# Performance work log

Measured on AMD Instinct MI355X. Metric: run time of the kernel, lower is better.

Reference implementation:

```python
import jax, jax.numpy as jnp
import numpy as np

B, S, D, H = 4, 2048, 1024, 16
DH = D // H
DFF = 4 * D
EPS = 1e-7


def _layernorm(x, scale, shift):
    # Note original quirk: (normalized + shift) * scale, biased variance, eps=1e-7
    m = jnp.mean(x, axis=-1, keepdims=True)
    v = jnp.mean((x - m) ** 2, axis=-1, keepdims=True)
    return ((x - m) / jnp.sqrt(v + EPS) + shift) * scale


def _gelu(x):
    c = jnp.sqrt(jnp.asarray(2.0 / jnp.pi, dtype=x.dtype))
    return 0.5 * x * (1.0 + jnp.tanh(c * (x + 0.044715 * x ** 3)))


def setup_inputs() -> dict:
    key = jax.random.key(0)
    ks = jax.random.split(key, 8)
    s = 0.02
    return {
        "x": jax.random.normal(ks[0], (B, S, D), jnp.float32),
        "Wq": jax.random.normal(ks[1], (D, D), jnp.float32) * s,
        "Wk": jax.random.normal(ks[2], (D, D), jnp.float32) * s,
        "Wv": jax.random.normal(ks[3], (D, D), jnp.float32) * s,
        "Wo": jax.random.normal(ks[4], (D, D), jnp.float32) * s,
        "bo": jnp.zeros((D,), jnp.float32),
        "W1": jax.random.normal(ks[5], (DFF, D), jnp.float32) * s,
        "b1": jnp.zeros((DFF,), jnp.float32),
        "W2": jax.random.normal(ks[6], (D, DFF), jnp.float32) * s,
        "b2": jnp.zeros((D,), jnp.float32),
        "ln1_scale": jnp.ones((D,), jnp.float32),
        "ln1_shift": jnp.zeros((D,), jnp.float32),
        "ln2_scale": jnp.ones((D,), jnp.float32),
        "ln2_shift": jnp.zeros((D,), jnp.float32),
    }


def reference(x, Wq, Wk, Wv, Wo, bo, W1, b1, W2, b2,
              ln1_scale, ln1_shift, ln2_scale, ln2_shift):
    b, s, d = x.shape
    h = _layernorm(x, ln1_scale, ln1_shift)
    # torch Linear: y = h @ W.T
    q = (h @ Wq.T).reshape(b, s, H, DH).transpose(0, 2, 1, 3)  # bhsd
    k = (h @ Wk.T).reshape(b, s, H, DH).transpose(0, 2, 1, 3)
    v = (h @ Wv.T).reshape(b, s, H, DH).transpose(0, 2, 1, 3)
    scores = jnp.einsum('bhqd,bhkd->bhqk', q, k) / jnp.sqrt(jnp.asarray(DH, x.dtype))
    causal = jnp.tril(jnp.ones((s, s), dtype=bool))
    scores = jnp.where(causal, scores, -jnp.inf)
    attn = jax.nn.softmax(scores, axis=-1)
    ctx = jnp.einsum('bhqk,bhkd->bhqd', attn, v)
    ctx = ctx.transpose(0, 2, 1, 3).reshape(b, s, d)
    attn_out = ctx @ Wo.T + bo
    x1 = x + attn_out  # residual (dropout is identity at eval / p effectively unused)
    h2 = _layernorm(x1, ln2_scale, ln2_shift)
    ff = _gelu(h2 @ W1.T + b1) @ W2.T + b2
    return x1 + ff
```

## Files before the change

kernel.cpp:

```cpp
#include <hip/hip_runtime.h>
#include <hip/hip_bf16.h>
#include <math.h>

typedef __bf16 bf16;
typedef __bf16 bf16x2_t __attribute__((ext_vector_type(2)));
typedef __bf16 bf16x4_t __attribute__((ext_vector_type(4)));
typedef __bf16 bf16x8_t __attribute__((ext_vector_type(8)));
typedef float  floatx4  __attribute__((ext_vector_type(4)));

#define DEVI static __device__ __forceinline__

constexpr int Bb = 4, Ss = 2048, Dd = 1024, Hh = 16, DHh = 64, DFFc = 4096;
constexpr int NTOK = Bb * Ss;
constexpr int NQKV = 3072;

DEVI void gld_lds16(const void* g, void* l) {
  __builtin_amdgcn_global_load_lds(
      (const __attribute__((address_space(1))) void*)g,
      (__attribute__((address_space(3))) void*)l, 16, 0, 0);
}

DEVI float gelu_f(float x) {
  const float c = 0.7978845608028654f;
  float t = tanhf(c * (x + 0.044715f * x * x * x));
  return 0.5f * x * (1.0f + t);
}

DEVI int xcd_lin(int lin, int nwg) {
  return (lin & 7) * (nwg >> 3) + (lin >> 3);
}

struct CastArgs {
  const float* src[6];
  bf16* dst[6];
  int n[6];
};
__global__ __launch_bounds__(256) void cast_w_kernel(CastArgs a) {
  const int which = blockIdx.y;
  const int idx = (blockIdx.x * 256 + threadIdx.x) * 4;
  if (idx >= a.n[which]) return;
  float4 v = *(const float4*)(a.src[which] + idx);
  bf16x4_t o = {(bf16)v.x, (bf16)v.y, (bf16)v.z, (bf16)v.w};
  *(bf16x4_t*)(a.dst[which] + idx) = o;
}

template <typename TIN>
__global__ __launch_bounds__(256) void ln_kernel(const TIN* __restrict__ x,
                                                 const float* __restrict__ sc,
                                                 const float* __restrict__ sh,
                                                 bf16* __restrict__ out) {
  __shared__ float rs[4], rs2[4];
  const int row = blockIdx.x, t = threadIdx.x;
  const TIN* xr = x + (size_t)row * Dd;
  float v[4];
  if constexpr (sizeof(TIN) == 2) {
    bf16x4_t tmp = *(const bf16x4_t*)((const bf16*)xr + t * 4);
#pragma unroll
    for (int i = 0; i < 4; i++) v[i] = (float)tmp[i];
  } else {
    float4 tmp = *(const float4*)((const float*)xr + t * 4);
    v[0] = tmp.x; v[1] = tmp.y; v[2] = tmp.z; v[3] = tmp.w;
  }
  float s = v[0] + v[1] + v[2] + v[3];
  float s2 = v[0] * v[0] + v[1] * v[1] + v[2] * v[2] + v[3] * v[3];
#pragma unroll
  for (int off = 1; off < 64; off <<= 1) {
    s += __shfl_xor(s, off);
    s2 += __shfl_xor(s2, off);
  }
  if ((t & 63) == 0) { rs[t >> 6] = s; rs2[t >> 6] = s2; }
  __syncthreads();
  float S1 = rs[0] + rs[1] + rs[2] + rs[3];
  float S2 = rs2[0] + rs2[1] + rs2[2] + rs2[3];
  float mean = S1 * (1.0f / Dd);
  float var = S2 * (1.0f / Dd) - mean * mean;
  float rinv = rsqrtf(var + 1e-7f);
#pragma unroll
  for (int i = 0; i < 4; i++) {
    int c = t * 4 + i;
    out[(size_t)row * Dd + c] = (bf16)(((v[i] - mean) * rinv + sh[c]) * sc[c]);
  }
}

template <int MODE>
__global__ __launch_bounds__(256) void gemm_bt(const bf16* __restrict__ A,
                                               const bf16* __restrict__ Bw,
                                               const float* __restrict__ bias,
                                               const void* __restrict__ res,
                                               void* __restrict__ outp,
                                               int M, int N, int K) {
  __shared__ bf16 As[128 * 32];
  __shared__ bf16 Bs[128 * 32];
  const int tid = threadIdx.x;
  const int gx = (int)gridDim.x;
  const int nwg = gx * (int)gridDim.y;
  const int lin = xcd_lin((int)blockIdx.y * gx + (int)blockIdx.x, nwg);
  const int m0 = (lin / gx) * 128;
  const int n0 = (lin % gx) * 128;
  const int wave = tid >> 6, lane = tid & 63;
  const int quad = lane >> 4, l16 = lane & 15;
  const int wm = (wave >> 1) * 64, wn = (wave & 1) * 64;

  floatx4 acc[4][4] = {};

  const int e0 = tid * 8;
  const int r0 = e0 >> 5, c0 = e0 & 31;
  const bf16* Ap0 = A + (size_t)(m0 + r0) * K + c0;
  const bf16* Ap1 = A + (size_t)(m0 + r0 + 64) * K + c0;
  const bf16* Bp0 = Bw + (size_t)(n0 + r0) * K + c0;
  const bf16* Bp1 = Bw + (size_t)(n0 + r0 + 64) * K + c0;

  for (int k = 0; k < K; k += 32) {
    __syncthreads();
    gld_lds16(Ap0 + k, As + e0);
    gld_lds16(Ap1 + k, As + e0 + 2048);
    gld_lds16(Bp0 + k, Bs + e0);
    gld_lds16(Bp1 + k, Bs + e0 + 2048);
    __syncthreads();

    bf16x8_t af[4], bfv[4];
#pragma unroll
    for (int i = 0; i < 4; i++) {
      af[i] = *(const bf16x8_t*)(As + (wm + i * 16 + l16) * 32 + quad * 8);
      bfv[i] = *(const bf16x8_t*)(Bs + (wn + i * 16 + l16) * 32 + quad * 8);
    }
#pragma unroll
    for (int i = 0; i < 4; i++)
#pragma unroll
      for (int j = 0; j < 4; j++)
        acc[i][j] =
            __builtin_amdgcn_mfma_f32_16x16x32_bf16(af[i], bfv[j], acc[i][j], 0, 0, 0);
  }

#pragma unroll
  for (int i = 0; i < 4; i++) {
    const int rbase = m0 + wm + i * 16 + quad * 4;
#pragma unroll
    for (int j = 0; j < 4; j++) {
      const int col = n0 + wn + j * 16 + l16;
      float bv = 0.f;
      if constexpr (MODE == 1 || MODE == 2 || MODE == 3) bv = bias[col];
#pragma unroll
      for (int r = 0; r < 4; r++) {
        const int row = rbase + r;
        float vacc = acc[i][j][r] + bv;
        if constexpr (MODE == 0) {
          ((bf16*)outp)[(size_t)row * N + col] = (bf16)vacc;
        } else if constexpr (MODE == 1) {
          float xres = ((const float*)res)[(size_t)row * N + col];
          ((bf16*)outp)[(size_t)row * N + col] = (bf16)(xres + vacc);
        } else if constexpr (MODE == 2) {
          ((bf16*)outp)[(size_t)row * N + col] = (bf16)gelu_f(vacc);
        } else {
          float xres = (float)((const bf16*)res)[(size_t)row * N + col];
          ((float*)outp)[(size_t)row * N + col] = xres + vacc;
        }
      }
    }
  }
}

__global__ __launch_bounds__(256) void attn_kernel(const bf16* __restrict__ QKV,
                                                   bf16* __restrict__ ctx) {
  __shared__ bf16 Ks[64 * 72];
  __shared__ bf16 Vt[64 * 72];
  __shared__ bf16 Ps[4][16 * 72];

  const int tid = threadIdx.x;
  const int wave = tid >> 6, lane = tid & 63;
  const int quad = lane >> 4, l16 = lane & 15;
  const int lin = xcd_lin((int)blockIdx.y * 16 + (int)blockIdx.x, 16 * Bb * Hh);
  const int qb = lin & 15;
  const int bh = lin >> 4;
  const int bsel = bh >> 4, hsel = bh & 15;
  const size_t base = ((size_t)bsel * Ss) * NQKV + (size_t)hsel * 64;
  const bf16* Qp = QKV + base;
  const bf16* Kp = QKV + base + 1024;
  const bf16* Vp = QKV + base + 2048;

  const int kr0 = tid >> 3, kc0 = (tid & 7) * 8;
  const int vp2 = tid & 31, vs = tid >> 5;

  for (int t = 0; t < 2; t++) {
    const int qt = (t == 0) ? qb : 31 - qb;
    const int q0 = qt * 64;

    const int qrow = q0 + wave * 16 + l16;
    bf16x8_t qf0 = *(const bf16x8_t*)(Qp + (size_t)qrow * NQKV + quad * 8);
    bf16x8_t qf1 = *(const bf16x8_t*)(Qp + (size_t)qrow * NQKV + 32 + quad * 8);
#pragma unroll
    for (int i = 0; i < 8; i++) {
      qf0[i] = (bf16)((float)qf0[i] * 0.125f);
      qf1[i] = (bf16)((float)qf1[i] * 0.125f);
    }

    floatx4 o[4] = {};
    float l_i[4] = {0.f, 0.f, 0.f, 0.f};

    for (int kc = 0; kc < q0 + 64; kc += 64) {
      __syncthreads();
      *(bf16x8_t*)(Ks + kr0 * 72 + kc0) =
          *(const bf16x8_t*)(Kp + (size_t)(kc + kr0) * NQKV + kc0);
      *(bf16x8_t*)(Ks + (kr0 + 32) * 72 + kc0) =
          *(const bf16x8_t*)(Kp + (size_t)(kc + kr0 + 32) * NQKV + kc0);
      {
        const bf16* v0p = Vp + (size_t)(kc + 2 * vp2) * NQKV + vs * 8;
        bf16x8_t va = *(const bf16x8_t*)(v0p);
        bf16x8_t vb = *(const bf16x8_t*)(v0p + NQKV);
#pragma unroll
        for (int i = 0; i < 8; i++) {
          bf16x2_t p2 = {va[i], vb[i]};
          *(bf16x2_t*)(Vt + (vs * 8 + i) * 72 + 2 * vp2) = p2;
        }
      }
      __syncthreads();

      floatx4 sg[4];
      __builtin_amdgcn_s_setprio(1);
#pragma unroll
      for (int g = 0; g < 4; g++) {
        floatx4 s = {0.f, 0.f, 0.f, 0.f};
        bf16x8_t ka = *(const bf16x8_t*)(Ks + (g * 16 + l16) * 72 + quad * 8);
        bf16x8_t kb = *(const bf16x8_t*)(Ks + (g * 16 + l16) * 72 + 32 + quad * 8);
        s = __builtin_amdgcn_mfma_f32_16x16x32_bf16(qf0, ka, s, 0, 0, 0);
        s = __builtin_amdgcn_mfma_f32_16x16x32_bf16(qf1, kb, s, 0, 0, 0);
        sg[g] = s;
      }
      __builtin_amdgcn_s_setprio(0);

      bf16* pw = &Ps[wave][0];
#pragma unroll
      for (int r = 0; r < 4; r++) {
        const int rq = q0 + wave * 16 + quad * 4 + r;
        float p[4];
        float rsum = 0.f;
#pragma unroll
        for (int g = 0; g < 4; g++) {
          float v = (kc + g * 16 + l16 > rq) ? -1e30f : sg[g][r];
          p[g] = __expf(v);
          rsum += p[g];
        }
        rsum += __shfl_xor(rsum, 1);
        rsum += __shfl_xor(rsum, 2);
        rsum += __shfl_xor(rsum, 4);
        rsum += __shfl_xor(rsum, 8);
        l_i[r] += rsum;
#pragma unroll
        for (int g = 0; g < 4; g++)
          pw[(quad * 4 + r) * 72 + g * 16 + l16] = (bf16)p[g];
      }
      __syncthreads();

      bf16x8_t pf0 = *(const bf16x8_t*)(pw + l16 * 72 + quad * 8);
      bf16x8_t pf1 = *(const bf16x8_t*)(pw + l16 * 72 + 32 + quad * 8);
      __builtin_amdgcn_s_setprio(1);
#pragma unroll
      for (int nt = 0; nt < 4; nt++) {
        bf16x8_t vf0 = *(const bf16x8_t*)(Vt + (nt * 16 + l16) * 72 + quad * 8);
        bf16x8_t vf1 = *(const bf16x8_t*)(Vt + (nt * 16 + l16) * 72 + 32 + quad * 8);
        o[nt] = __builtin_amdgcn_mfma_f32_16x16x32_bf16(pf0, vf0, o[nt], 0, 0, 0);
        o[nt] = __builtin_amdgcn_mfma_f32_16x16x32_bf16(pf1, vf1, o[nt], 0, 0, 0);
      }
      __builtin_amdgcn_s_setprio(0);
    }

#pragma unroll
    for (int nt = 0; nt < 4; nt++)
#pragma unroll
      for (int r = 0; r < 4; r++) {
        const int rq = q0 + wave * 16 + quad * 4 + r;
        size_t a = ((size_t)bsel * Ss + rq) * Dd + (size_t)hsel * DHh + nt * 16 + l16;
        ctx[a] = (bf16)(o[nt][r] / l_i[r]);
      }
  }
}

extern "C" void kernel_launch(void* const* d_in, const int* in_sizes, int n_in,
                              void* d_out, int out_size, void* d_ws, size_t ws_size,
                              hipStream_t stream) {
  (void)in_sizes; (void)n_in; (void)out_size; (void)ws_size;
  const float* x = (const float*)d_in[0];
  const float* Wq = (const float*)d_in[1];
  const float* Wk = (const float*)d_in[2];
  const float* Wv = (const float*)d_in[3];
  const float* Wo = (const float*)d_in[4];
  const float* bo = (const float*)d_in[5];
  const float* W1 = (const float*)d_in[6];
  const float* b1 = (const float*)d_in[7];
  const float* W2 = (const float*)d_in[8];
  const float* b2 = (const float*)d_in[9];
  const float* ln1s = (const float*)d_in[10];
  const float* ln1b = (const float*)d_in[11];
  const float* ln2s = (const float*)d_in[12];
  const float* ln2b = (const float*)d_in[13];

  char* wsb = (char*)d_ws;
  const size_t MB = 1024 * 1024;
  bf16* Wqb = (bf16*)(wsb);
  bf16* Wkb = (bf16*)(wsb + 2 * MB);
  bf16* Wvb = (bf16*)(wsb + 4 * MB);
  bf16* Wob = (bf16*)(wsb + 6 * MB);
  bf16* W1b = (bf16*)(wsb + 8 * MB);
  bf16* W2b = (bf16*)(wsb + 16 * MB);
  bf16* h   = (bf16*)(wsb + 24 * MB);
  bf16* qkv = (bf16*)(wsb + 40 * MB);
  bf16* ctx = (bf16*)(wsb + 88 * MB);
  bf16* x1  = (bf16*)(wsb + 104 * MB);
  bf16* h2  = ctx;
  bf16* ff1 = h;

  dim3 blk(256, 1, 1);

  CastArgs ca;
  ca.src[0] = Wq; ca.src[1] = Wk; ca.src[2] = Wv; ca.src[3] = Wo;
  ca.src[4] = W1; ca.src[5] = W2;
  ca.dst[0] = Wqb; ca.dst[1] = Wkb; ca.dst[2] = Wvb; ca.dst[3] = Wob;
  ca.dst[4] = W1b; ca.dst[5] = W2b;
  ca.n[0] = ca.n[1] = ca.n[2] = ca.n[3] = Dd * Dd;
  ca.n[4] = ca.n[5] = Dd * DFFc;
  cast_w_kernel<<<dim3((Dd * DFFc) / (256 * 4), 6, 1), blk, 0, stream>>>(ca);

  ln_kernel<float><<<dim3(NTOK, 1, 1), blk, 0, stream>>>(x, ln1s, ln1b, h);
  gemm_bt<0><<<dim3(24, NTOK / 128, 1), blk, 0, stream>>>(h, Wqb, nullptr, nullptr, qkv,
                                                          NTOK, NQKV, Dd);
  attn_kernel<<<dim3(16, Bb * Hh, 1), blk, 0, stream>>>(qkv, ctx);
  gemm_bt<1><<<dim3(8, NTOK / 128, 1), blk, 0, stream>>>(ctx, Wob, bo, x, x1, NTOK, Dd, Dd);
  ln_kernel<bf16><<<dim3(NTOK, 1, 1), blk, 0, stream>>>(x1, ln2s, ln2b, h2);
  gemm_bt<2><<<dim3(32, NTOK / 128, 1), blk, 0, stream>>>(h2, W1b, b1, nullptr, ff1, NTOK,
                                                          DFFc, Dd);
  gemm_bt<3><<<dim3(8, NTOK / 128, 1), blk, 0, stream>>>(ff1, W2b, b2, x1, (float*)d_out,
                                                         NTOK, Dd, DFFc);
}
```

Before: 558.1 us.

## Replace GEMMs with 8-wave double-buffered swizzled-LDS kernel using 256-row tiles

Replaces the simple 128x128, K=32 single-buffered GEMM with a 512-thread kernel using 256xBN tiles and K=64 steps. LDS is double-buffered so the next tile's global-to-LDS loads are issued in phases while MFMAs run on the current buffer. An XOR swizzle is applied to the LDS layout to avoid bank conflicts. Wave priority is raised around the MFMA blocks. The larger tiles and LDS footprint reduce occupancy and grid size, and the GEMMs for smaller N now launch fewer workgroups.

After: 521.9 us. -6.5%, faster.

```diff
diff --git a/kernel.cpp b/kernel.cpp
--- a/kernel.cpp
+++ b/kernel.cpp
@@ -82,68 +82,154 @@
   }
 }
 
-template <int MODE>
-__global__ __launch_bounds__(256) void gemm_bt(const bf16* __restrict__ A,
-                                               const bf16* __restrict__ Bw,
-                                               const float* __restrict__ bias,
-                                               const void* __restrict__ res,
-                                               void* __restrict__ outp,
-                                               int M, int N, int K) {
-  __shared__ bf16 As[128 * 32];
-  __shared__ bf16 Bs[128 * 32];
+template <int BN, int MODE>
+__global__ __launch_bounds__(512, 2) void gemm8(const bf16* __restrict__ A,
+                                                const bf16* __restrict__ Bw,
+                                                const float* __restrict__ bias,
+                                                const void* __restrict__ res,
+                                                void* __restrict__ outp,
+                                                int M, int N, int K) {
+  constexpr int WARPS_N = (BN == 256) ? 4 : 2;
+  constexpr int WR_H = (BN == 256) ? 128 : 64;
+  constexpr int M_rep = WR_H / 16;
+  constexpr int MPP = M_rep / 4;
+  constexpr int NBCH = BN / 128;
+  constexpr int BELEM = BN * 64;
+  __shared__ bf16 lds[32768 + 2 * BELEM];
+
   const int tid = threadIdx.x;
+  const int w = tid >> 6, lane = tid & 63;
+  const int quad = lane >> 4, l16 = lane & 15;
+  const int l7x8 = (lane & 7) << 3;
+  const int wr = w / WARPS_N, wc = w % WARPS_N;
+
   const int gx = (int)gridDim.x;
   const int nwg = gx * (int)gridDim.y;
   const int lin = xcd_lin((int)blockIdx.y * gx + (int)blockIdx.x, nwg);
-  const int m0 = (lin / gx) * 128;
-  const int n0 = (lin % gx) * 128;
-  const int wave = tid >> 6, lane = tid & 63;
-  const int quad = lane >> 4, l16 = lane & 15;
-  const int wm = (wave >> 1) * 64, wn = (wave & 1) * 64;
-
-  floatx4 acc[4][4] = {};
-
-  const int e0 = tid * 8;
-  const int r0 = e0 >> 5, c0 = e0 & 31;
-  const bf16* Ap0 = A + (size_t)(m0 + r0) * K + c0;
-  const bf16* Ap1 = A + (size_t)(m0 + r0 + 64) * K + c0;
-  const bf16* Bp0 = Bw + (size_t)(n0 + r0) * K + c0;
-  const bf16* Bp1 = Bw + (size_t)(n0 + r0 + 64) * K + c0;
-
-  for (int k = 0; k < K; k += 32) {
-    __syncthreads();
-    gld_lds16(Ap0 + k, As + e0);
-    gld_lds16(Ap1 + k, As + e0 + 2048);
-    gld_lds16(Bp0 + k, Bs + e0);
-    gld_lds16(Bp1 + k, Bs + e0 + 2048);
-    __syncthreads();
-
-    bf16x8_t af[4], bfv[4];
-#pragma unroll
-    for (int i = 0; i < 4; i++) {
-      af[i] = *(const bf16x8_t*)(As + (wm + i * 16 + l16) * 32 + quad * 8);
-      bfv[i] = *(const bf16x8_t*)(Bs + (wn + i * 16 + l16) * 32 + quad * 8);
+  const int m0 = (lin / gx) * 256;
+  const int n0 = (lin % gx) * BN;
+
+  const int s0 = w * 1024 + lane * 16;
+  const int sr = s0 >> 7;
+  const int sc = ((s0 ^ ((sr & 7) << 4)) & 127) >> 1;
+  const int toff = w * 512 + lane * 8;
+
+  const bf16* Ag[2][2];
+  const bf16* Bg[NBCH][2];
+#pragma unroll
+  for (int h = 0; h < 2; h++)
+#pragma unroll
+    for (int j = 0; j < 2; j++)
+      Ag[h][j] = A + (size_t)(m0 + h * 128 + sr + j * 64) * K + sc;
+#pragma unroll
+  for (int h = 0; h < NBCH; h++)
+#pragma unroll
+    for (int j = 0; j < 2; j++)
+      Bg[h][j] = Bw + (size_t)(n0 + h * 128 + sr + j * 64) * K + sc;
+
+  const int abase = (wr * WR_H + l16) * 64 + quad * 8;
+  const int bbase = (wc * 64 + l16) * 64 + quad * 8;
+
+  floatx4 acc[M_rep][4] = {};
+
+#pragma unroll
+  for (int h = 0; h < 2; h++)
+#pragma unroll
+    for (int j = 0; j < 2; j++)
+      gld_lds16(Ag[h][j], lds + h * 8192 + j * 4096 + toff);
+#pragma unroll
+  for (int h = 0; h < NBCH; h++)
+#pragma unroll
+    for (int j = 0; j < 2; j++)
+      gld_lds16(Bg[h][j], lds + 32768 + h * 8192 + j * 4096 + toff);
+  asm volatile("s_waitcnt vmcnt(0)" ::: "memory");
+  __builtin_amdgcn_s_barrier();
+  __builtin_amdgcn_sched_barrier(0);
+
+  const int NT = K >> 6;
+  int koff = 64;
+  for (int t = 0; t < NT; ++t) {
+    const int q = t & 1;
+    const int aq = q * 16384;
+    const int bq = 32768 + q * BELEM;
+    const int aqn = (q ^ 1) * 16384;
+    const int bqn = 32768 + (q ^ 1) * BELEM;
+    const bool st = (t + 1) < NT;
+
+    bf16x8_t bfr[4][2];
+#pragma unroll
+    for (int p = 0; p < 4; ++p) {
+      if (st) {
+        if (p == 0) {
+#pragma unroll
+          for (int j = 0; j < 2; j++)
+            gld_lds16(Ag[0][j] + koff, lds + aqn + j * 4096 + toff);
+#pragma unroll
+          for (int j = 0; j < 2; j++)
+            gld_lds16(Bg[0][j] + koff, lds + bqn + j * 4096 + toff);
+        }
+        if (p == 1) {
+#pragma unroll
+          for (int j = 0; j < 2; j++)
+            gld_lds16(Ag[1][j] + koff, lds + aqn + 8192 + j * 4096 + toff);
+        }
+        if (p == 2 && NBCH == 2) {
+#pragma unroll
+          for (int j = 0; j < 2; j++)
+            gld_lds16(Bg[1][j] + koff, lds + bqn + 8192 + j * 4096 + toff);
+        }
+      }
+      bf16x8_t af[MPP][2];
+#pragma unroll
+      for (int im = 0; im < MPP; ++im)
+#pragma unroll
+        for (int kk = 0; kk < 2; ++kk)
+          af[im][kk] = *(const bf16x8_t*)(
+              lds + aq + ((abase + (p * MPP + im) * 1024 + kk * 32) ^ l7x8));
+      if (p == 0) {
+#pragma unroll
+        for (int j2 = 0; j2 < 4; ++j2)
+#pragma unroll
+          for (int kk = 0; kk < 2; ++kk)
+            bfr[j2][kk] = *(const bf16x8_t*)(
+                lds + bq + ((bbase + j2 * 1024 + kk * 32) ^ l7x8));
+      }
+      __builtin_amdgcn_s_barrier();
+      __builtin_amdgcn_sched_barrier(0);
+      __builtin_amdgcn_s_setprio(1);
+#pragma unroll
+      for (int im = 0; im < MPP; ++im)
+#pragma unroll
+        for (int j2 = 0; j2 < 4; ++j2)
+#pragma unroll
+          for (int kk = 0; kk < 2; ++kk)
+            acc[p * MPP + im][j2] = __builtin_amdgcn_mfma_f32_16x16x32_bf16(
+                af[im][kk], bfr[j2][kk], acc[p * MPP + im][j2], 0, 0, 0);
+      __builtin_amdgcn_s_setprio(0);
+      if (p < 3) {
+        __builtin_amdgcn_s_barrier();
+        __builtin_amdgcn_sched_barrier(0);
+      }
     }
-#pragma unroll
-    for (int i = 0; i < 4; i++)
-#pragma unroll
-      for (int j = 0; j < 4; j++)
-        acc[i][j] =
-            __builtin_amdgcn_mfma_f32_16x16x32_bf16(af[i], bfv[j], acc[i][j], 0, 0, 0);
-  }
-
-#pragma unroll
-  for (int i = 0; i < 4; i++) {
-    const int rbase = m0 + wm + i * 16 + quad * 4;
-#pragma unroll
-    for (int j = 0; j < 4; j++) {
-      const int col = n0 + wn + j * 16 + l16;
+    asm volatile("s_waitcnt vmcnt(0)" ::: "memory");
+    __builtin_amdgcn_sched_barrier(0);
+    __builtin_amdgcn_s_barrier();
+    __builtin_amdgcn_sched_barrier(0);
+    if (st) koff += 64;
+  }
+
+#pragma unroll
+  for (int i = 0; i < M_rep; ++i) {
+    const int rbase = m0 + wr * WR_H + i * 16 + quad * 4;
+#pragma unroll
+    for (int j2 = 0; j2 < 4; ++j2) {
+      const int col = n0 + wc * 64 + j2 * 16 + l16;
       float bv = 0.f;
       if constexpr (MODE == 1 || MODE == 2 || MODE == 3) bv = bias[col];
 #pragma unroll
-      for (int r = 0; r < 4; r++) {
+      for (int r = 0; r < 4; ++r) {
         const int row = rbase + r;
-        float vacc = acc[i][j][r] + bv;
+        float vacc = acc[i][j2][r] + bv;
         if constexpr (MODE == 0) {
           ((bf16*)outp)[(size_t)row * N + col] = (bf16)vacc;
         } else if constexpr (MODE == 1) {
@@ -310,6 +396,7 @@
   bf16* ff1 = h;
 
   dim3 blk(256, 1, 1);
+  dim3 blk8(512, 1, 1);
 
   CastArgs ca;
   ca.src[0] = Wq; ca.src[1] = Wk; ca.src[2] = Wv; ca.src[3] = Wo;
@@ -321,13 +408,14 @@
   cast_w_kernel<<<dim3((Dd * DFFc) / (256 * 4), 6, 1), blk, 0, stream>>>(ca);
 
   ln_kernel<float><<<dim3(NTOK, 1, 1), blk, 0, stream>>>(x, ln1s, ln1b, h);
-  gemm_bt<0><<<dim3(24, NTOK / 128, 1), blk, 0, stream>>>(h, Wqb, nullptr, nullptr, qkv,
-                                                          NTOK, NQKV, Dd);
+  gemm8<128, 0><<<dim3(24, NTOK / 256, 1), blk8, 0, stream>>>(h, Wqb, nullptr, nullptr,
+                                                              qkv, NTOK, NQKV, Dd);
   attn_kernel<<<dim3(16, Bb * Hh, 1), blk, 0, stream>>>(qkv, ctx);
-  gemm_bt<1><<<dim3(8, NTOK / 128, 1), blk, 0, stream>>>(ctx, Wob, bo, x, x1, NTOK, Dd, Dd);
+  gemm8<128, 1><<<dim3(8, NTOK / 256, 1), blk8, 0, stream>>>(ctx, Wob, bo, x, x1,
+                                                             NTOK, Dd, Dd);
   ln_kernel<bf16><<<dim3(NTOK, 1, 1), blk, 0, stream>>>(x1, ln2s, ln2b, h2);
-  gemm_bt<2><<<dim3(32, NTOK / 128, 1), blk, 0, stream>>>(h2, W1b, b1, nullptr, ff1, NTOK,
-                                                          DFFc, Dd);
-  gemm_bt<3><<<dim3(8, NTOK / 128, 1), blk, 0, stream>>>(ff1, W2b, b2, x1, (float*)d_out,
-                                                         NTOK, Dd, DFFc);
-}
+  gemm8<256, 2><<<dim3(16, NTOK / 256, 1), blk8, 0, stream>>>(h2, W1b, b1, nullptr, ff1,
+                                                              NTOK, DFFc, Dd);
+  gemm8<128, 3><<<dim3(8, NTOK / 256, 1), blk8, 0, stream>>>(ff1, W2b, b2, x1,
+                                                             (float*)d_out, NTOK, Dd, DFFc);
+}
```
